# Kernel tuning notes

Hardware: AMD Instinct MI355X
Metric: run time of the kernel (lower is better)

The kernel has to match this reference:

```python
import jax, jax.numpy as jnp
import numpy as np
import math

B, S, D_IN, EMBED, H = 4, 1024, 1024, 1024, 16
HD = EMBED // H  # 64


def setup_inputs() -> dict:
    key = jax.random.key(0)
    ks = jax.random.split(key, 8)
    x = jax.random.normal(ks[0], (B, S, D_IN), dtype=jnp.float32)
    mask = jax.random.randint(ks[1], (B, S, S), 0, 2, dtype=jnp.int32)
    weights = jax.random.uniform(ks[2], (B, S, S), dtype=jnp.float32)
    # xavier-uniform-ish scale for projections
    lim_qkv = math.sqrt(6.0 / (D_IN + 3 * EMBED))
    lim_o = math.sqrt(6.0 / (EMBED + EMBED))
    W_qkv = jax.random.uniform(ks[3], (3 * EMBED, D_IN), minval=-lim_qkv, maxval=lim_qkv, dtype=jnp.float32)
    b_qkv = jnp.zeros((3 * EMBED,), dtype=jnp.float32)
    W_o = jax.random.uniform(ks[4], (EMBED, EMBED), minval=-lim_o, maxval=lim_o, dtype=jnp.float32)
    b_o = jnp.zeros((EMBED,), dtype=jnp.float32)
    return {"x": x, "mask": mask, "weights": weights, "W_qkv": W_qkv, "b_qkv": b_qkv, "W_o": W_o, "b_o": b_o}


def reference(x, mask, weights, W_qkv, b_qkv, W_o, b_o):
    b, s, _ = x.shape
    # QKV projection: [b, s, 3*EMBED] -> [b, H, s, 3*HD]
    qkv = (x @ W_qkv.T + b_qkv).reshape(b, s, H, 3 * HD).transpose(0, 2, 1, 3)
    q, k, v = jnp.split(qkv, 3, axis=-1)  # each [b, H, s, HD]
    logits = jnp.einsum('bhqd,bhkd->bhqk', q, k) / math.sqrt(HD)
    logits = jnp.where(mask[:, None, :, :] == 0, jnp.float32(-9e15), logits)
    # weights transposed on last two dims, broadcast over heads
    w = jnp.swapaxes(weights, -2, -1)[:, None, :, :]  # [b, 1, s, s]
    m = jnp.max(logits, axis=-1, keepdims=True)
    e = w * jnp.exp(logits - m)
    attn = e / jnp.sum(e, axis=-1, keepdims=True)
    vals = jnp.einsum('bhqk,bhkd->bhqd', attn, v)
    vals = vals.transpose(0, 2, 1, 3).reshape(b, s, EMBED)
    return vals @ W_o.T + b_o
```

## Files before the change

kernel.cpp:

```cpp
#include <hip/hip_runtime.h>
#include <hip/hip_bf16.h>
#include <stdint.h>

#define SDIM 1024
#define BATCH 4
#define NH 16
#define HDIM 64
#define KDIM 1024
#define N_QKV 3072
#define EMB 1024

typedef uint16_t u16;
typedef __attribute__((ext_vector_type(4))) float f32x4;
typedef __attribute__((ext_vector_type(8))) short bf16x8;
typedef __attribute__((ext_vector_type(8))) unsigned short u16x8;

__device__ __forceinline__ u16 f2bf(float f) {
  union { float f; uint32_t u; } x; x.f = f;
  uint32_t r = x.u + 0x7FFFu + ((x.u >> 16) & 1u);
  return (u16)(r >> 16);
}

__device__ __forceinline__ float bf2f(u16 b) {
  union { uint32_t u; float f; } x; x.u = ((uint32_t)b) << 16;
  return x.f;
}

__device__ __forceinline__ void gload_lds16(const u16* g, u16* l) {
  __builtin_amdgcn_global_load_lds(
      (const __attribute__((address_space(1))) unsigned int*)g,
      (__attribute__((address_space(3))) unsigned int*)l, 16, 0, 0);
}

#define N8_X  524288
#define N8_WQ 393216
#define N8_WO 131072
__global__ void cvt3_kernel(const float* __restrict__ a, const float* __restrict__ b,
                            const float* __restrict__ c,
                            u16* __restrict__ oa, u16* __restrict__ ob, u16* __restrict__ oc) {
  const int total = N8_X + N8_WQ + N8_WO;
  int stride = gridDim.x * blockDim.x;
  for (int i = blockIdx.x * blockDim.x + threadIdx.x; i < total; i += stride) {
    const float* s; u16* d; int j;
    if (i < N8_X)            { s = a; d = oa; j = i; }
    else if (i < N8_X + N8_WQ){ s = b; d = ob; j = i - N8_X; }
    else                     { s = c; d = oc; j = i - N8_X - N8_WQ; }
    const float4* s4 = (const float4*)s + (size_t)j * 2;
    float4 u = s4[0], v = s4[1];
    u16x8 o;
    o[0] = f2bf(u.x); o[1] = f2bf(u.y); o[2] = f2bf(u.z); o[3] = f2bf(u.w);
    o[4] = f2bf(v.x); o[5] = f2bf(v.y); o[6] = f2bf(v.z); o[7] = f2bf(v.w);
    ((u16x8*)d)[j] = o;
  }
}

__global__ __launch_bounds__(512, 2) void gemm_qkv_wm3(
    const u16* __restrict__ A, const u16* __restrict__ Bm,
    const float* __restrict__ bias,
    u16* __restrict__ Qh, u16* __restrict__ Kh, u16* __restrict__ Vt,
    const int* __restrict__ mask, const float* __restrict__ wts, u16* __restrict__ wm3)
{
  __shared__ char smem[131072];
  const int tid = threadIdx.x;

  if (blockIdx.x < 192) {
    const int gid = blockIdx.x;
    const int brow = (gid & 15) * 256, bcol = (gid >> 4) * 256;
    const int wid = tid >> 6, lane = tid & 63;
    const int g = lane >> 4, c = lane & 15, cx = c & 7;
    const int wr = wid >> 2, wc = wid & 3;

    const u16* asrc[4]; const u16* bsrc[4]; int doff[4];
    #pragma unroll
    for (int j = 0; j < 4; ++j) {
      int i = j * 512 + tid;
      int row = i >> 3, sch = (i & 7) ^ (row & 7);
      asrc[j] = A  + (size_t)(brow + row) * KDIM + sch * 8;
      bsrc[j] = Bm + (size_t)(bcol + row) * KDIM + sch * 8;
      doff[j] = (j * 512 + wid * 64) * 16;
    }

    auto stage = [&](int kt, int slot) {
      char* base = smem + slot * 65536;
      #pragma unroll
      for (int j = 0; j < 4; ++j)
        gload_lds16(asrc[j] + kt * 64, (u16*)(base + doff[j]));
      #pragma unroll
      for (int j = 0; j < 4; ++j)
        gload_lds16(bsrc[j] + kt * 64, (u16*)(base + 32768 + doff[j]));
    };

    f32x4 acc[8][4] = {};

    stage(0, 0);
    __syncthreads();

    for (int kt = 0; kt < 16; ++kt) {
      if (kt < 15) stage(kt + 1, (kt + 1) & 1);

      const char* As = smem + (kt & 1) * 65536;
      const char* Bs = As + 32768;

      #pragma unroll
      for (int kk = 0; kk < 2; ++kk) {
        bf16x8 af[8], bfr[4];
        #pragma unroll
        for (int m = 0; m < 8; ++m) {
          int row = wr * 128 + m * 16 + c;
          af[m] = *(const bf16x8*)(As + (row << 7) + ((((kk << 2) + g) ^ cx) << 4));
        }
        #pragma unroll
        for (int n = 0; n < 4; ++n) {
          int row = wc * 64 + n * 16 + c;
          bfr[n] = *(const bf16x8*)(Bs + (row << 7) + ((((kk << 2) + g) ^ cx) << 4));
        }
        __builtin_amdgcn_s_setprio(1);
        #pragma unroll
        for (int m = 0; m < 8; ++m)
          #pragma unroll
          for (int n = 0; n < 4; ++n)
            acc[m][n] = __builtin_amdgcn_mfma_f32_16x16x32_bf16(
                af[m], bfr[n], acc[m][n], 0, 0, 0);
        __builtin_amdgcn_s_setprio(0);
      }
      __syncthreads();
    }

    #pragma unroll
    for (int m = 0; m < 8; ++m) {
      #pragma unroll
      for (int n = 0; n < 4; ++n) {
        int col = bcol + wc * 64 + n * 16 + c;
        float bv = bias[col];
        int h = col / 192;
        int rem = col - h * 192;
        int sec = rem >> 6, d = rem & 63;
        #pragma unroll
        for (int r = 0; r < 4; ++r) {
          int row = brow + wr * 128 + m * 16 + g * 4 + r;
          int b = row >> 10, sl = row & 1023;
          float v = acc[m][n][r] + bv;
          if (sec == 0)
            Qh[((size_t)(b * NH + h) * SDIM + sl) * HDIM + d] = f2bf(v * 0.125f);
          else if (sec == 1)
            Kh[((size_t)(b * NH + h) * SDIM + sl) * HDIM + d] = f2bf(v);
          else
            Vt[((size_t)(b * NH + h) * HDIM + d) * SDIM + sl] = f2bf(v);
        }
      }
    }
  } else {
    const int wmid = blockIdx.x - 192;
    const size_t SS = (size_t)SDIM * SDIM;
    int   (*mt)[69] = (int(*)[69])smem;
    float (*wt)[69] = (float(*)[69])(smem + 17664);

    #pragma unroll
    for (int tt = 0; tt < 2; ++tt) {
      const int id = wmid * 2 + tt;
      const int kt = id & 15, qt = (id >> 4) & 15, b = id >> 8;
      const int q0 = qt * 64, k0 = kt * 64;
      if (tt) __syncthreads();

      #pragma unroll
      for (int j = 0; j < 2; ++j) {
        int idx = j * 512 + tid;
        int row = idx >> 4, c4 = idx & 15;
        int4 m4 = *(const int4*)(mask + (size_t)b * SS + (size_t)(q0 + row) * SDIM + k0 + c4 * 4);
        mt[row][c4 * 4 + 0] = m4.x; mt[row][c4 * 4 + 1] = m4.y;
        mt[row][c4 * 4 + 2] = m4.z; mt[row][c4 * 4 + 3] = m4.w;
        float4 w4 = *(const float4*)(wts + (size_t)b * SS + (size_t)(k0 + row) * SDIM + q0 + c4 * 4);
        wt[row][c4 * 4 + 0] = w4.x; wt[row][c4 * 4 + 1] = w4.y;
        wt[row][c4 * 4 + 2] = w4.z; wt[row][c4 * 4 + 3] = w4.w;
      }
      __syncthreads();

      const int wid2 = tid >> 7, hf = (tid >> 6) & 1, lane = tid & 63;
      const int g2 = lane >> 4, c2 = lane & 15;
      const int ql = wid2 * 16 + c2;
      u16x8 o;
      #pragma unroll
      for (int e = 0; e < 8; ++e) {
        int kl = 8 * g2 + 4 * (e >> 2) + (e & 3) + 32 * hf;
        o[e] = mt[ql][kl] ? f2bf(wt[kl][ql]) : (u16)0;
      }
      size_t off = ((((size_t)(b * 16 + qt) * 4 + wid2) * 16 + kt)) * 1024 + lane * 16 + hf * 8;
      *(u16x8*)(wm3 + off) = o;
    }
  }
}

__global__ __launch_bounds__(256) void gemm_bt(
    const u16* __restrict__ A, const u16* __restrict__ Bm,
    const float* __restrict__ bias, float* __restrict__ C,
    int M, int N, int K)
{
  __shared__ u16 As[128 * 64];
  __shared__ u16 Bs[128 * 64];
  const int tid = threadIdx.x;
  const int wid = tid >> 6, lane = tid & 63;
  const int g = lane >> 4, c = lane & 15, cx = c & 7;
  const int wrow = (wid >> 1) * 64, wcol = (wid & 1) * 64;
  const int brow = blockIdx.x * 128, bcol = blockIdx.y * 128;

  const u16* asrc[4]; const u16* bsrc[4]; u16* adst[4]; u16* bdst[4];
  #pragma unroll
  for (int j = 0; j < 4; ++j) {
    int ci = j * 256 + tid;
    int row = ci >> 3, sch = (ci & 7) ^ (row & 7);
    asrc[j] = A  + (size_t)(brow + row) * K + sch * 8;
    bsrc[j] = Bm + (size_t)(bcol + row) * K + sch * 8;
    adst[j] = As + (j * 256 + wid * 64) * 8;
    bdst[j] = Bs + (j * 256 + wid * 64) * 8;
  }

  f32x4 acc[4][4] = {};
  const char* Asc = (const char*)As;
  const char* Bsc = (const char*)Bs;

  for (int kt = 0; kt < K / 64; ++kt) {
    #pragma unroll
    for (int j = 0; j < 4; ++j) {
      gload_lds16(asrc[j] + kt * 64, adst[j]);
      gload_lds16(bsrc[j] + kt * 64, bdst[j]);
    }
    __syncthreads();

    bf16x8 af[2][4], bfr[2][4];
    #pragma unroll
    for (int kk = 0; kk < 2; ++kk)
      #pragma unroll
      for (int i = 0; i < 4; ++i) {
        int cha = ((kk << 2) + g) ^ cx;
        af[kk][i]  = *(const bf16x8*)(Asc + ((wrow + i * 16 + c) << 7) + (cha << 4));
        bfr[kk][i] = *(const bf16x8*)(Bsc + ((wcol + i * 16 + c) << 7) + (cha << 4));
      }
    #pragma unroll
    for (int kk = 0; kk < 2; ++kk)
      #pragma unroll
      for (int mi = 0; mi < 4; ++mi)
        #pragma unroll
        for (int ni = 0; ni < 4; ++ni)
          acc[mi][ni] = __builtin_amdgcn_mfma_f32_16x16x32_bf16(
              af[kk][mi], bfr[kk][ni], acc[mi][ni], 0, 0, 0);
    __syncthreads();
  }

  #pragma unroll
  for (int mi = 0; mi < 4; ++mi)
    #pragma unroll
    for (int ni = 0; ni < 4; ++ni) {
      int col = bcol + wcol + ni * 16 + c;
      float bv = bias[col];
      #pragma unroll
      for (int r = 0; r < 4; ++r) {
        int row = brow + wrow + mi * 16 + g * 4 + r;
        C[(size_t)row * N + col] = acc[mi][ni][r] + bv;
      }
    }
}

__global__ __launch_bounds__(256, 4) void attn_kernel(
    const u16* __restrict__ Qh, const u16* __restrict__ Kh, const u16* __restrict__ Vt,
    const u16* __restrict__ wm3, u16* __restrict__ vals)
{
  int bid = blockIdx.x;
  int swz = (bid & 7) * 128 + (bid >> 3);
  const int qt = swz & 15, bh = swz >> 4;
  const int h = bh & 15, b = bh >> 4;

  const int tid = threadIdx.x;
  const int wid = tid >> 6, lane = tid & 63;
  const int g = lane >> 4, c = lane & 15;
  const int qloc = qt * 64 + wid * 16;

  __shared__ u16 Kb[2][4096];
  __shared__ u16 Vb[2][4096];

  const u16* qp = Qh + ((size_t)bh * SDIM + qloc + c) * HDIM;
  bf16x8 qa0 = *(const bf16x8*)(qp + g * 8);
  bf16x8 qa1 = *(const bf16x8*)(qp + 32 + g * 8);

  const u16* kbase = Kh + (size_t)bh * SDIM * HDIM;
  const u16* vbase = Vt + (size_t)bh * HDIM * SDIM;
  const u16* wbase = wm3 + (((size_t)(b * 16 + qt) * 4 + wid) * 16) * 1024 + lane * 16;

  float l_run = 0.f;
  f32x4 acc_o[4] = {};

  auto fsw = [](int row) { return ((row ^ (row >> 3)) & 7) ^ ((row & 1) << 2); };

  int kro[4], kxr[4], vro[4], vxr[4];
  #pragma unroll
  for (int st = 0; st < 4; ++st) {
    int kr = ((c >> 2) << 3) + ((st & 1) << 2) + (c & 3) + ((st >> 1) << 5);
    kro[st] = kr << 7;
    kxr[st] = fsw(kr);
  }
  #pragma unroll
  for (int dt = 0; dt < 4; ++dt) {
    int vr = dt * 16 + c;
    vro[dt] = vr << 7;
    vxr[dt] = fsw(vr);
  }

  auto stage = [&](int buf, int kt) {
    const int k0 = kt * 64;
    #pragma unroll
    for (int j = 0; j < 2; ++j) {
      int i = j * 256 + tid;
      int row = i >> 3;
      int sch = (i & 7) ^ (((row ^ (row >> 3)) & 7) ^ ((row & 1) << 2));
      gload_lds16(kbase + (size_t)(k0 + row) * HDIM + sch * 8,
                  &Kb[buf][(size_t)(j * 256 + wid * 64) * 8]);
      gload_lds16(vbase + (size_t)row * SDIM + k0 + sch * 8,
                  &Vb[buf][(size_t)(j * 256 + wid * 64) * 8]);
    }
  };

  stage(0, 0);
  __syncthreads();
  int cur = 0;

  for (int kt = 0; kt < 16; ++kt) {
    if (kt < 15) stage(cur ^ 1, kt + 1);

    u16x8 w0 = *(const u16x8*)(wbase + kt * 1024);
    u16x8 w1 = *(const u16x8*)(wbase + kt * 1024 + 8);

    const char* kb = (const char*)&Kb[cur][0];
    const char* vb = (const char*)&Vb[cur][0];

    f32x4 sc[4];
    #pragma unroll
    for (int st = 0; st < 4; ++st) {
      bf16x8 ka0 = *(const bf16x8*)(kb + kro[st] + ((g ^ kxr[st]) << 4));
      bf16x8 ka1 = *(const bf16x8*)(kb + kro[st] + (((4 + g) ^ kxr[st]) << 4));
      f32x4 z = {};
      z = __builtin_amdgcn_mfma_f32_16x16x32_bf16(ka0, qa0, z, 0, 0, 0);
      z = __builtin_amdgcn_mfma_f32_16x16x32_bf16(ka1, qa1, z, 0, 0, 0);
      sc[st] = z;
    }

    float p[4][4];
    #pragma unroll
    for (int st = 0; st < 4; ++st) {
      #pragma unroll
      for (int r = 0; r < 4; ++r) {
        u16 wv = (st < 2) ? ((const u16*)&w0)[st * 4 + r]
                          : ((const u16*)&w1)[(st - 2) * 4 + r];
        float pv = bf2f(wv) * __expf(sc[st][r]);
        p[st][r] = pv;
        l_run += pv;
      }
    }

    uint32_t pk[8];
    #pragma unroll
    for (int i = 0; i < 8; ++i) {
      float lo = p[i >> 1][(i & 1) * 2], hi = p[i >> 1][(i & 1) * 2 + 1];
      asm("v_cvt_pk_bf16_f32 %0, %1, %2" : "=v"(pk[i]) : "v"(lo), "v"(hi));
    }
    union PA { uint32_t u[4]; bf16x8 v; } a0, a1;
    #pragma unroll
    for (int i = 0; i < 4; ++i) { a0.u[i] = pk[i]; a1.u[i] = pk[4 + i]; }

    #pragma unroll
    for (int dt = 0; dt < 4; ++dt) {
      bf16x8 vb0 = *(const bf16x8*)(vb + vro[dt] + ((g ^ vxr[dt]) << 4));
      bf16x8 vb1 = *(const bf16x8*)(vb + vro[dt] + (((4 + g) ^ vxr[dt]) << 4));
      acc_o[dt] = __builtin_amdgcn_mfma_f32_16x16x32_bf16(a0.v, vb0, acc_o[dt], 0, 0, 0);
      acc_o[dt] = __builtin_amdgcn_mfma_f32_16x16x32_bf16(a1.v, vb1, acc_o[dt], 0, 0, 0);
    }

    __syncthreads();
    cur ^= 1;
  }

  l_run += __shfl_xor(l_run, 16);
  l_run += __shfl_xor(l_run, 32);

  float inv[4];
  #pragma unroll
  for (int r = 0; r < 4; ++r)
    inv[r] = 1.0f / __shfl(l_run, g * 4 + r);

  #pragma unroll
  for (int dt = 0; dt < 4; ++dt)
    #pragma unroll
    for (int r = 0; r < 4; ++r) {
      int row = b * SDIM + qloc + g * 4 + r;
      vals[(size_t)row * EMB + h * HDIM + dt * 16 + c] = f2bf(acc_o[dt][r] * inv[r]);
    }
}

extern "C" void kernel_launch(void* const* d_in, const int* in_sizes, int n_in,
                              void* d_out, int out_size, void* d_ws, size_t ws_size,
                              hipStream_t stream) {
  const float* x     = (const float*)d_in[0];
  const int*   mask  = (const int*)d_in[1];
  const float* wts   = (const float*)d_in[2];
  const float* W_qkv = (const float*)d_in[3];
  const float* b_qkv = (const float*)d_in[4];
  const float* W_o   = (const float*)d_in[5];
  const float* b_o   = (const float*)d_in[6];
  float* out = (float*)d_out;

  char* ws = (char*)d_ws;
  u16* xb   = (u16*)(ws);
  u16* wqb  = (u16*)(ws + (8ull  << 20));
  u16* wob  = (u16*)(ws + (14ull << 20));
  u16* Qh   = (u16*)(ws + (16ull << 20));
  u16* Kh   = (u16*)(ws + (24ull << 20));
  u16* Vt   = (u16*)(ws + (32ull << 20));
  u16* valb = (u16*)(ws + (40ull << 20));
  u16* wm3b = (u16*)d_out;

  cvt3_kernel<<<2048, 256, 0, stream>>>(x, W_qkv, W_o, xb, wqb, wob);

  gemm_qkv_wm3<<<704, 512, 0, stream>>>(xb, wqb, b_qkv, Qh, Kh, Vt, mask, wts, wm3b);

  attn_kernel<<<1024, 256, 0, stream>>>(Qh, Kh, Vt, wm3b, valb);

  dim3 g3(32, 8);
  gemm_bt<<<g3, 256, 0, stream>>>(valb, wob, b_o, out, BATCH * SDIM, EMB, KDIM);
}
```

Before: 108.5 us.

## Retile QKV GEMM to 256x192 and fuse mask-weight prep into every block

The QKV GEMM moves from 192 blocks of 256x256 tiles to 256 blocks of 256x192 tiles, which matches the 256 compute units and gives each block one whole head's 192 columns. Each block now also handles four mask/weight tiles, previously spread over 512 separate blocks. The first GEMM stage is issued asynchronously before that prep work, so the prep overlaps with the first global-to-LDS load. The trade-off is less reuse per tile, occupancy dropping to one block per CU, and serial prep time added in front of the GEMM in every block.

```diff
diff --git a/kernel.cpp b/kernel.cpp
--- a/kernel.cpp
+++ b/kernel.cpp
@@ -54,7 +54,7 @@
   }
 }
 
-__global__ __launch_bounds__(512, 2) void gemm_qkv_wm3(
+__global__ __launch_bounds__(512, 1) void gemm_qkv_wm3(
     const u16* __restrict__ A, const u16* __restrict__ Bm,
     const float* __restrict__ bias,
     u16* __restrict__ Qh, u16* __restrict__ Kh, u16* __restrict__ Vt,
@@ -62,102 +62,49 @@
 {
   __shared__ char smem[131072];
   const int tid = threadIdx.x;
-
-  if (blockIdx.x < 192) {
-    const int gid = blockIdx.x;
-    const int brow = (gid & 15) * 256, bcol = (gid >> 4) * 256;
-    const int wid = tid >> 6, lane = tid & 63;
-    const int g = lane >> 4, c = lane & 15, cx = c & 7;
-    const int wr = wid >> 2, wc = wid & 3;
-
-    const u16* asrc[4]; const u16* bsrc[4]; int doff[4];
-    #pragma unroll
-    for (int j = 0; j < 4; ++j) {
-      int i = j * 512 + tid;
-      int row = i >> 3, sch = (i & 7) ^ (row & 7);
-      asrc[j] = A  + (size_t)(brow + row) * KDIM + sch * 8;
-      bsrc[j] = Bm + (size_t)(bcol + row) * KDIM + sch * 8;
-      doff[j] = (j * 512 + wid * 64) * 16;
-    }
-
-    auto stage = [&](int kt, int slot) {
-      char* base = smem + slot * 65536;
-      #pragma unroll
-      for (int j = 0; j < 4; ++j)
-        gload_lds16(asrc[j] + kt * 64, (u16*)(base + doff[j]));
-      #pragma unroll
-      for (int j = 0; j < 4; ++j)
-        gload_lds16(bsrc[j] + kt * 64, (u16*)(base + 32768 + doff[j]));
-    };
-
-    f32x4 acc[8][4] = {};
-
-    stage(0, 0);
-    __syncthreads();
-
-    for (int kt = 0; kt < 16; ++kt) {
-      if (kt < 15) stage(kt + 1, (kt + 1) & 1);
-
-      const char* As = smem + (kt & 1) * 65536;
-      const char* Bs = As + 32768;
-
-      #pragma unroll
-      for (int kk = 0; kk < 2; ++kk) {
-        bf16x8 af[8], bfr[4];
-        #pragma unroll
-        for (int m = 0; m < 8; ++m) {
-          int row = wr * 128 + m * 16 + c;
-          af[m] = *(const bf16x8*)(As + (row << 7) + ((((kk << 2) + g) ^ cx) << 4));
-        }
-        #pragma unroll
-        for (int n = 0; n < 4; ++n) {
-          int row = wc * 64 + n * 16 + c;
-          bfr[n] = *(const bf16x8*)(Bs + (row << 7) + ((((kk << 2) + g) ^ cx) << 4));
-        }
-        __builtin_amdgcn_s_setprio(1);
-        #pragma unroll
-        for (int m = 0; m < 8; ++m)
-          #pragma unroll
-          for (int n = 0; n < 4; ++n)
-            acc[m][n] = __builtin_amdgcn_mfma_f32_16x16x32_bf16(
-                af[m], bfr[n], acc[m][n], 0, 0, 0);
-        __builtin_amdgcn_s_setprio(0);
-      }
-      __syncthreads();
-    }
-
-    #pragma unroll
-    for (int m = 0; m < 8; ++m) {
-      #pragma unroll
-      for (int n = 0; n < 4; ++n) {
-        int col = bcol + wc * 64 + n * 16 + c;
-        float bv = bias[col];
-        int h = col / 192;
-        int rem = col - h * 192;
-        int sec = rem >> 6, d = rem & 63;
-        #pragma unroll
-        for (int r = 0; r < 4; ++r) {
-          int row = brow + wr * 128 + m * 16 + g * 4 + r;
-          int b = row >> 10, sl = row & 1023;
-          float v = acc[m][n][r] + bv;
-          if (sec == 0)
-            Qh[((size_t)(b * NH + h) * SDIM + sl) * HDIM + d] = f2bf(v * 0.125f);
-          else if (sec == 1)
-            Kh[((size_t)(b * NH + h) * SDIM + sl) * HDIM + d] = f2bf(v);
-          else
-            Vt[((size_t)(b * NH + h) * HDIM + d) * SDIM + sl] = f2bf(v);
-        }
-      }
-    }
-  } else {
-    const int wmid = blockIdx.x - 192;
+  const int gid = blockIdx.x;
+  const int brow = (gid & 15) * 256, bcol = (gid >> 4) * 192;
+  const int wid = tid >> 6, lane = tid & 63;
+  const int g = lane >> 4, c = lane & 15, cx = c & 7;
+  const int wr = wid & 3, wc = wid >> 2;
+
+  const u16* asrc[4]; int adoff[4];
+  #pragma unroll
+  for (int j = 0; j < 4; ++j) {
+    int i = j * 512 + tid;
+    int row = i >> 3, sch = (i & 7) ^ (row & 7);
+    asrc[j] = A + (size_t)(brow + row) * KDIM + sch * 8;
+    adoff[j] = (j * 512 + wid * 64) * 16;
+  }
+  const u16* bsrc[3]; int bdoff[3];
+  #pragma unroll
+  for (int j = 0; j < 3; ++j) {
+    int i = j * 512 + tid;
+    int row = i >> 3, sch = (i & 7) ^ (row & 7);
+    bsrc[j] = Bm + (size_t)(bcol + row) * KDIM + sch * 8;
+    bdoff[j] = 32768 + (j * 512 + wid * 64) * 16;
+  }
+
+  auto stage = [&](int kt, int slot) {
+    char* base = smem + slot * 57344;
+    #pragma unroll
+    for (int j = 0; j < 4; ++j)
+      gload_lds16(asrc[j] + kt * 64, (u16*)(base + adoff[j]));
+    #pragma unroll
+    for (int j = 0; j < 3; ++j)
+      gload_lds16(bsrc[j] + kt * 64, (u16*)(base + bdoff[j]));
+  };
+
+  stage(0, 0);
+
+  {
     const size_t SS = (size_t)SDIM * SDIM;
-    int   (*mt)[69] = (int(*)[69])smem;
-    float (*wt)[69] = (float(*)[69])(smem + 17664);
-
-    #pragma unroll
-    for (int tt = 0; tt < 2; ++tt) {
-      const int id = wmid * 2 + tt;
+    int   (*mt)[69] = (int(*)[69])(smem + 57344);
+    float (*wt)[69] = (float(*)[69])(smem + 57344 + 17664);
+
+    #pragma unroll
+    for (int tt = 0; tt < 4; ++tt) {
+      const int id = gid * 4 + tt;
       const int kt = id & 15, qt = (id >> 4) & 15, b = id >> 8;
       const int q0 = qt * 64, k0 = kt * 64;
       if (tt) __syncthreads();
@@ -175,8 +122,8 @@
       }
       __syncthreads();
 
-      const int wid2 = tid >> 7, hf = (tid >> 6) & 1, lane = tid & 63;
-      const int g2 = lane >> 4, c2 = lane & 15;
+      const int wid2 = tid >> 7, hf = (tid >> 6) & 1, lane2 = tid & 63;
+      const int g2 = lane2 >> 4, c2 = lane2 & 15;
       const int ql = wid2 * 16 + c2;
       u16x8 o;
       #pragma unroll
@@ -184,8 +131,66 @@
         int kl = 8 * g2 + 4 * (e >> 2) + (e & 3) + 32 * hf;
         o[e] = mt[ql][kl] ? f2bf(wt[kl][ql]) : (u16)0;
       }
-      size_t off = ((((size_t)(b * 16 + qt) * 4 + wid2) * 16 + kt)) * 1024 + lane * 16 + hf * 8;
+      size_t off = ((((size_t)(b * 16 + qt) * 4 + wid2) * 16 + kt)) * 1024 + lane2 * 16 + hf * 8;
       *(u16x8*)(wm3 + off) = o;
+    }
+    __syncthreads();
+  }
+
+  f32x4 acc[4][6] = {};
+
+  for (int kt = 0; kt < 16; ++kt) {
+    if (kt < 15) stage(kt + 1, (kt + 1) & 1);
+
+    const char* As = smem + (kt & 1) * 57344;
+    const char* Bs = As + 32768;
+
+    #pragma unroll
+    for (int kk = 0; kk < 2; ++kk) {
+      bf16x8 af[4], bfr[6];
+      #pragma unroll
+      for (int m = 0; m < 4; ++m) {
+        int row = wr * 64 + m * 16 + c;
+        af[m] = *(const bf16x8*)(As + (row << 7) + ((((kk << 2) + g) ^ cx) << 4));
+      }
+      #pragma unroll
+      for (int n = 0; n < 6; ++n) {
+        int row = wc * 96 + n * 16 + c;
+        bfr[n] = *(const bf16x8*)(Bs + (row << 7) + ((((kk << 2) + g) ^ cx) << 4));
+      }
+      __builtin_amdgcn_s_setprio(1);
+      #pragma unroll
+      for (int m = 0; m < 4; ++m)
+        #pragma unroll
+        for (int n = 0; n < 6; ++n)
+          acc[m][n] = __builtin_amdgcn_mfma_f32_16x16x32_bf16(
+              af[m], bfr[n], acc[m][n], 0, 0, 0);
+      __builtin_amdgcn_s_setprio(0);
+    }
+    __syncthreads();
+  }
+
+  #pragma unroll
+  for (int m = 0; m < 4; ++m) {
+    #pragma unroll
+    for (int n = 0; n < 6; ++n) {
+      int col = bcol + wc * 96 + n * 16 + c;
+      float bv = bias[col];
+      int h = col / 192;
+      int rem = col - h * 192;
+      int sec = rem >> 6, d = rem & 63;
+      #pragma unroll
+      for (int r = 0; r < 4; ++r) {
+        int row = brow + wr * 64 + m * 16 + g * 4 + r;
+        int b = row >> 10, sl = row & 1023;
+        float v = acc[m][n][r] + bv;
+        if (sec == 0)
+          Qh[((size_t)(b * NH + h) * SDIM + sl) * HDIM + d] = f2bf(v * 0.125f);
+        else if (sec == 1)
+          Kh[((size_t)(b * NH + h) * SDIM + sl) * HDIM + d] = f2bf(v);
+        else
+          Vt[((size_t)(b * NH + h) * HDIM + d) * SDIM + sl] = f2bf(v);
+      }
     }
   }
 }
@@ -418,7 +423,7 @@
 
   cvt3_kernel<<<2048, 256, 0, stream>>>(x, W_qkv, W_o, xb, wqb, wob);
 
-  gemm_qkv_wm3<<<704, 512, 0, stream>>>(xb, wqb, b_qkv, Qh, Kh, Vt, mask, wts, wm3b);
+  gemm_qkv_wm3<<<256, 512, 0, stream>>>(xb, wqb, b_qkv, Qh, Kh, Vt, mask, wts, wm3b);
 
   attn_kernel<<<1024, 256, 0, stream>>>(Qh, Kh, Vt, wm3b, valb);
 
```

Result: no change. 106.8 us (-1.6%).
